# Performance work log

Hardware: AMD Instinct MI355X
Metric: run time of the kernel (lower is better)

The kernel has to match this reference:

```python
import jax, jax.numpy as jnp
import numpy as np

IN_DIM = 64
OUT_DIM = 16  # SPD matrix side
HIDDEN = [128, 128]
CHOL_DIM = OUT_DIM + OUT_DIM * (OUT_DIM - 1) // 2  # 136
BATCH = 65536
LEAKY_SLOPE = 0.01  # torch.nn.LeakyReLU default


def _uniform(key, shape, in_feat):
    b = 1.0 / in_feat
    return jax.random.uniform(key, shape, jnp.float32, -b, b)


def setup_inputs() -> dict:
    key = jax.random.key(0)
    ks = jax.random.split(key, 7)
    x = jax.random.normal(ks[0], (BATCH, IN_DIM), jnp.float32)
    # layer sizes: 64 -> 128 -> 128 -> 136, init uniform(-1/in_feat, 1/in_feat)
    W1 = _uniform(ks[1], (IN_DIM, HIDDEN[0]), IN_DIM)
    b1 = _uniform(ks[2], (HIDDEN[0],), IN_DIM)
    W2 = _uniform(ks[3], (HIDDEN[0], HIDDEN[1]), HIDDEN[0])
    b2 = _uniform(ks[4], (HIDDEN[1],), HIDDEN[0])
    W3 = _uniform(ks[5], (HIDDEN[1], CHOL_DIM), HIDDEN[1])
    b3 = _uniform(ks[6], (CHOL_DIM,), HIDDEN[1])
    return {"x": x, "W1": W1, "b1": b1, "W2": W2, "b2": b2, "W3": W3, "b3": b3}


def reference(x, W1, b1, W2, b2, W3, b3):
    # MLP with LeakyReLU between layers, then Tanh on final output
    h = jax.nn.leaky_relu(x @ W1 + b1, LEAKY_SLOPE)
    h = jax.nn.leaky_relu(h @ W2 + b2, LEAKY_SLOPE)
    ldata = jnp.tanh(h @ W3 + b3)  # [B, 136]

    # fill_tril: scatter the 136 values into the lower triangle (row-major)
    rows, cols = jnp.tril_indices(OUT_DIM)
    L = jnp.zeros((x.shape[0], OUT_DIM, OUT_DIM), x.dtype).at[:, rows, cols].set(ldata)
    Q = L + jnp.swapaxes(L, -1, -2)  # symmetric [B, 16, 16]

    # symmetric eigendecomposition (ascending eigenvalues, like torch.symeig)
    w, V = jnp.linalg.eigh(Q)
    # sqrt(softmax(exp(w)**2)) ; exp(w)**2 == exp(2w)
    ev = jnp.sqrt(jax.nn.softmax(jnp.exp(2.0 * w), axis=-1))  # [B, 16]
    # faithful to source: uses inverse (== V^T in exact math since V orthogonal)
    Vinv = jnp.linalg.inv(V)
    # V @ diag(ev) @ V^{-1}
    return jnp.einsum('bij,bj,bjk->bik', V, ev, Vinv)
```

## Files before the change

kernel.cpp:

```cpp
#include <hip/hip_runtime.h>
#include <math.h>

typedef _Float16 f16;
typedef _Float16 half4_t __attribute__((ext_vector_type(4)));
typedef _Float16 half8_t __attribute__((ext_vector_type(8)));
typedef float floatx4 __attribute__((ext_vector_type(4)));

#define LDATA_OFF_BYTES 86016

__global__ __launch_bounds__(256) void prep_weights(
    const float* __restrict__ W1, const float* __restrict__ W2,
    const float* __restrict__ W3, f16* __restrict__ wt) {
  int t = blockIdx.x * 256 + threadIdx.x;
  if (t < 8192) {
    int c = t >> 6, k = t & 63;
    wt[t] = (f16)W1[k * 128 + c];
  } else if (t < 24576) {
    int u = t - 8192;
    int c = u >> 7, k = u & 127;
    wt[t] = (f16)W2[k * 128 + c];
  } else if (t < 43008) {
    int u = t - 24576;
    int c = u >> 7, k = u & 127;
    wt[t] = (f16)((c < 136) ? W3[k * 136 + c] : 0.0f);
  }
}

__device__ __forceinline__ float fast_tanh(float v) {
  float e = __builtin_amdgcn_exp2f(v * 2.885390081777926814f);
  return 1.0f - 2.0f * __builtin_amdgcn_rcpf(e + 1.0f);
}

__global__ __launch_bounds__(256) void mlp_kernel(
    const float* __restrict__ x, const float* __restrict__ b1,
    const float* __restrict__ b2v, const float* __restrict__ b3,
    const f16* __restrict__ wt, f16* __restrict__ ldata) {
  __shared__ f16 hb[2][4][16][136];
  const int tid = threadIdx.x;
  const int wave = tid >> 6;
  const int lane = tid & 63;
  const int cl = lane & 15;
  const int q = lane >> 4;
  const int r0 = blockIdx.x * 64 + wave * 16;

  const f16* w1t = wt;
  const f16* w2t = wt + 8192;
  const f16* w3t = wt + 24576;

  half8_t a0, a1;
  {
    const float* xr = x + (size_t)(r0 + cl) * 64 + q * 8;
    floatx4 v0 = *(const floatx4*)(xr);
    floatx4 v1 = *(const floatx4*)(xr + 4);
    floatx4 v2 = *(const floatx4*)(xr + 32);
    floatx4 v3 = *(const floatx4*)(xr + 36);
#pragma unroll
    for (int i = 0; i < 4; ++i) {
      a0[i] = (f16)v0[i]; a0[i + 4] = (f16)v1[i];
      a1[i] = (f16)v2[i]; a1[i + 4] = (f16)v3[i];
    }
  }
#pragma unroll
  for (int c8 = 0; c8 < 8; ++c8) {
    int c = c8 * 16 + cl;
    half8_t w0 = *(const half8_t*)(w1t + c * 64 + q * 8);
    half8_t w1v = *(const half8_t*)(w1t + c * 64 + 32 + q * 8);
    floatx4 acc = {0.f, 0.f, 0.f, 0.f};
    acc = __builtin_amdgcn_mfma_f32_16x16x32_f16(a0, w0, acc, 0, 0, 0);
    acc = __builtin_amdgcn_mfma_f32_16x16x32_f16(a1, w1v, acc, 0, 0, 0);
    float bias = b1[c];
#pragma unroll
    for (int i = 0; i < 4; ++i) {
      float v = acc[i] + bias;
      v = v > 0.f ? v : 0.01f * v;
      hb[0][wave][q * 4 + i][c] = (f16)v;
    }
  }
  __syncthreads();

  half8_t ha[4];
#pragma unroll
  for (int ks = 0; ks < 4; ++ks)
    ha[ks] = *(const half8_t*)(&hb[0][wave][cl][ks * 32 + q * 8]);
#pragma unroll
  for (int c8 = 0; c8 < 8; ++c8) {
    int c = c8 * 16 + cl;
    floatx4 acc = {0.f, 0.f, 0.f, 0.f};
#pragma unroll
    for (int ks = 0; ks < 4; ++ks) {
      half8_t wv = *(const half8_t*)(w2t + c * 128 + ks * 32 + q * 8);
      acc = __builtin_amdgcn_mfma_f32_16x16x32_f16(ha[ks], wv, acc, 0, 0, 0);
    }
    float bias = b2v[c];
#pragma unroll
    for (int i = 0; i < 4; ++i) {
      float v = acc[i] + bias;
      v = v > 0.f ? v : 0.01f * v;
      hb[1][wave][q * 4 + i][c] = (f16)v;
    }
  }
  __syncthreads();

#pragma unroll
  for (int ks = 0; ks < 4; ++ks)
    ha[ks] = *(const half8_t*)(&hb[1][wave][cl][ks * 32 + q * 8]);
#pragma unroll
  for (int c8 = 0; c8 < 9; ++c8) {
    int c = c8 * 16 + cl;
    floatx4 acc = {0.f, 0.f, 0.f, 0.f};
#pragma unroll
    for (int ks = 0; ks < 4; ++ks) {
      half8_t wv = *(const half8_t*)(w3t + c * 128 + ks * 32 + q * 8);
      acc = __builtin_amdgcn_mfma_f32_16x16x32_f16(ha[ks], wv, acc, 0, 0, 0);
    }
    if (c < 136) {
      float bias = b3[c];
#pragma unroll
      for (int i = 0; i < 4; ++i)
        ldata[(size_t)(r0 + q * 4 + i) * 136 + c] = (f16)fast_tanh(acc[i] + bias);
    }
  }
}

template <int CTRL>
__device__ __forceinline__ float dpp_add(float v) {
  int t = __builtin_amdgcn_update_dpp(0, __builtin_bit_cast(int, v), CTRL,
                                      0xf, 0xf, true);
  return v + __builtin_bit_cast(float, t);
}
__device__ __forceinline__ float wsum(float v) {
  v = dpp_add<0x111>(v);
  v = dpp_add<0x112>(v);
  v = dpp_add<0x114>(v);
  v = dpp_add<0x118>(v);
  v = dpp_add<0x142>(v);
  v = dpp_add<0x143>(v);
  return __builtin_bit_cast(
      float, __builtin_amdgcn_readlane(__builtin_bit_cast(int, v), 63));
}

__device__ __forceinline__ half4_t to_h(floatx4 v) {
  auto p0 = __builtin_amdgcn_cvt_pkrtz(v[0], v[1]);
  auto p1 = __builtin_amdgcn_cvt_pkrtz(v[2], v[3]);
  half4_t h;
  h[0] = p0[0]; h[1] = p0[1]; h[2] = p1[0]; h[3] = p1[1];
  return h;
}

__device__ __forceinline__ floatx4 expm_c(floatx4 b, floatx4 I4, float& m) {
  float s2 = wsum(b[0] * b[0] + b[1] * b[1] + b[2] * b[2] + b[3] * b[3]);
  float td = wsum(I4[0] * b[0] + I4[1] * b[1] + I4[2] * b[2] + I4[3] * b[3]);
  m = td * 0.0625f;
  float fr2 = fmaxf(s2 - td * m, 1e-30f);
  int e2 = (int)(__builtin_bit_cast(unsigned, fr2) >> 23) - 127;
  int s = (e2 + 5) >> 1;
  s = s < 0 ? 0 : (s > 12 ? 12 : s);
  s = __builtin_amdgcn_readfirstlane(s);
  float sc = __builtin_bit_cast(float, (unsigned)(127 - s) << 23);
  b = (b - I4 * m) * sc;
  half4_t bh = to_h(b);
  floatx4 zero = {0.f, 0.f, 0.f, 0.f};
  floatx4 a2 = __builtin_amdgcn_mfma_f32_16x16x16f16(bh, bh, zero, 0, 0, 0);
  floatx4 t = I4 * 0.5f + b * (1.f / 6.f) + a2 * (1.f / 24.f);
  floatx4 p = __builtin_amdgcn_mfma_f32_16x16x16f16(to_h(a2), to_h(t), I4 + b,
                                                    0, 0, 0);
  for (int k = 0; k < s; ++k) {
    half4_t ph = to_h(p);
    p = __builtin_amdgcn_mfma_f32_16x16x16f16(ph, ph, zero, 0, 0, 0);
  }
  return p;
}

__global__ __launch_bounds__(256) void expm_kernel(
    const f16* __restrict__ ldata, float* __restrict__ out) {
  const int lane = threadIdx.x & 63;
  const int mat = (int)((blockIdx.x * 256u + threadIdx.x) >> 6);
  const int r = lane & 15, q = lane >> 4;
  const f16* ld = ldata + (size_t)mat * 136;

  floatx4 b, I4;
#pragma unroll
  for (int i = 0; i < 4; ++i) {
    int k = q * 4 + i;
    int hi = r > k ? r : k;
    int lo = r + k - hi;
    float v = (float)ld[hi * (hi + 1) / 2 + lo];
    bool d = (r == k);
    I4[i] = d ? 1.f : 0.f;
    b[i] = d ? 4.f * v : 2.f * v;
  }

  float m1;
  floatx4 p = expm_c(b, I4, m1);
  float fac = __builtin_amdgcn_exp2f(m1 * 1.4426950408889634f - 1.0f);
  float m2;
  p = expm_c(p * fac, I4, m2);

  float n2 = wsum(p[0] * p[0] + p[1] * p[1] + p[2] * p[2] + p[3] * p[3]);
  float inv = __builtin_amdgcn_rsqf(n2);
  floatx4 o = p * inv;
  *(floatx4*)(out + (size_t)mat * 256 + r * 16 + q * 4) = o;
}

extern "C" void kernel_launch(void* const* d_in, const int* in_sizes, int n_in,
                              void* d_out, int out_size, void* d_ws,
                              size_t ws_size, hipStream_t stream) {
  const float* x = (const float*)d_in[0];
  const float* W1 = (const float*)d_in[1];
  const float* b1 = (const float*)d_in[2];
  const float* W2 = (const float*)d_in[3];
  const float* b2 = (const float*)d_in[4];
  const float* W3 = (const float*)d_in[5];
  const float* b3 = (const float*)d_in[6];
  float* out = (float*)d_out;
  f16* wt = (f16*)d_ws;
  f16* ldata = (f16*)((char*)d_ws + LDATA_OFF_BYTES);

  prep_weights<<<168, 256, 0, stream>>>(W1, W2, W3, wt);
  mlp_kernel<<<1024, 256, 0, stream>>>(x, b1, b2, b3, wt, ldata);
  expm_kernel<<<16384, 256, 0, stream>>>(ldata, out);
}
```

Before: 148.9 us.

## Keep MLP weights in registers and loop each wave over four row tiles

The MLP kernel now runs one wave per block. That wave keeps the W2/W3 fragments and biases in registers and processes four 16-row tiles in a loop, prefetching the next tile's x. Activations go through a small XOR-swizzled LDS buffer, with no block barriers, to avoid bank conflicts. This removes repeated global/L2 weight loads per tile, at the cost of very high register pressure (68 half8 fragments) and lower occupancy with only 1024 single-wave blocks.

```diff
diff --git a/kernel.cpp b/kernel.cpp
--- a/kernel.cpp
+++ b/kernel.cpp
@@ -31,93 +31,126 @@
   return 1.0f - 2.0f * __builtin_amdgcn_rcpf(e + 1.0f);
 }
 
-__global__ __launch_bounds__(256) void mlp_kernel(
+__global__ __launch_bounds__(64, 1) void mlp_kernel(
     const float* __restrict__ x, const float* __restrict__ b1,
     const float* __restrict__ b2v, const float* __restrict__ b3,
     const f16* __restrict__ wt, f16* __restrict__ ldata) {
-  __shared__ f16 hb[2][4][16][136];
-  const int tid = threadIdx.x;
-  const int wave = tid >> 6;
-  const int lane = tid & 63;
+  __shared__ f16 act[2048];
+  const int lane = threadIdx.x & 63;
   const int cl = lane & 15;
   const int q = lane >> 4;
-  const int r0 = blockIdx.x * 64 + wave * 16;
-
   const f16* w1t = wt;
   const f16* w2t = wt + 8192;
   const f16* w3t = wt + 24576;
 
-  half8_t a0, a1;
-  {
-    const float* xr = x + (size_t)(r0 + cl) * 64 + q * 8;
-    floatx4 v0 = *(const floatx4*)(xr);
-    floatx4 v1 = *(const floatx4*)(xr + 4);
-    floatx4 v2 = *(const floatx4*)(xr + 32);
-    floatx4 v3 = *(const floatx4*)(xr + 36);
+  half8_t w2f[32], w3f[36];
+#pragma unroll
+  for (int c8 = 0; c8 < 8; ++c8) {
+    int c = c8 * 16 + cl;
+#pragma unroll
+    for (int ks = 0; ks < 4; ++ks)
+      w2f[c8 * 4 + ks] = *(const half8_t*)(w2t + c * 128 + ks * 32 + q * 8);
+  }
+#pragma unroll
+  for (int c8 = 0; c8 < 9; ++c8) {
+    int c = c8 * 16 + cl;
+#pragma unroll
+    for (int ks = 0; ks < 4; ++ks)
+      w3f[c8 * 4 + ks] = *(const half8_t*)(w3t + c * 128 + ks * 32 + q * 8);
+  }
+  float bb1[8], bb2[8], bb3[9];
+#pragma unroll
+  for (int c8 = 0; c8 < 8; ++c8) {
+    bb1[c8] = b1[c8 * 16 + cl];
+    bb2[c8] = b2v[c8 * 16 + cl];
+    bb3[c8] = b3[c8 * 16 + cl];
+  }
+  bb3[8] = (cl < 8) ? b3[128 + cl] : 0.f;
+
+  const int tile0 = blockIdx.x * 4;
+  const float* xp = x + (size_t)(tile0 * 16 + cl) * 64 + q * 8;
+  floatx4 v0 = *(const floatx4*)xp;
+  floatx4 v1 = *(const floatx4*)(xp + 4);
+  floatx4 v2 = *(const floatx4*)(xp + 32);
+  floatx4 v3 = *(const floatx4*)(xp + 36);
+
+  for (int t = 0; t < 4; ++t) {
+    const int r0 = (tile0 + t) * 16;
+    half8_t a0, a1;
 #pragma unroll
     for (int i = 0; i < 4; ++i) {
       a0[i] = (f16)v0[i]; a0[i + 4] = (f16)v1[i];
       a1[i] = (f16)v2[i]; a1[i + 4] = (f16)v3[i];
     }
-  }
-#pragma unroll
-  for (int c8 = 0; c8 < 8; ++c8) {
-    int c = c8 * 16 + cl;
-    half8_t w0 = *(const half8_t*)(w1t + c * 64 + q * 8);
-    half8_t w1v = *(const half8_t*)(w1t + c * 64 + 32 + q * 8);
-    floatx4 acc = {0.f, 0.f, 0.f, 0.f};
-    acc = __builtin_amdgcn_mfma_f32_16x16x32_f16(a0, w0, acc, 0, 0, 0);
-    acc = __builtin_amdgcn_mfma_f32_16x16x32_f16(a1, w1v, acc, 0, 0, 0);
-    float bias = b1[c];
-#pragma unroll
-    for (int i = 0; i < 4; ++i) {
-      float v = acc[i] + bias;
-      v = v > 0.f ? v : 0.01f * v;
-      hb[0][wave][q * 4 + i][c] = (f16)v;
-    }
-  }
-  __syncthreads();
-
-  half8_t ha[4];
-#pragma unroll
-  for (int ks = 0; ks < 4; ++ks)
-    ha[ks] = *(const half8_t*)(&hb[0][wave][cl][ks * 32 + q * 8]);
-#pragma unroll
-  for (int c8 = 0; c8 < 8; ++c8) {
-    int c = c8 * 16 + cl;
-    floatx4 acc = {0.f, 0.f, 0.f, 0.f};
-#pragma unroll
-    for (int ks = 0; ks < 4; ++ks) {
-      half8_t wv = *(const half8_t*)(w2t + c * 128 + ks * 32 + q * 8);
-      acc = __builtin_amdgcn_mfma_f32_16x16x32_f16(ha[ks], wv, acc, 0, 0, 0);
-    }
-    float bias = b2v[c];
-#pragma unroll
-    for (int i = 0; i < 4; ++i) {
-      float v = acc[i] + bias;
-      v = v > 0.f ? v : 0.01f * v;
-      hb[1][wave][q * 4 + i][c] = (f16)v;
-    }
-  }
-  __syncthreads();
-
-#pragma unroll
-  for (int ks = 0; ks < 4; ++ks)
-    ha[ks] = *(const half8_t*)(&hb[1][wave][cl][ks * 32 + q * 8]);
-#pragma unroll
-  for (int c8 = 0; c8 < 9; ++c8) {
-    int c = c8 * 16 + cl;
-    floatx4 acc = {0.f, 0.f, 0.f, 0.f};
-#pragma unroll
-    for (int ks = 0; ks < 4; ++ks) {
-      half8_t wv = *(const half8_t*)(w3t + c * 128 + ks * 32 + q * 8);
-      acc = __builtin_amdgcn_mfma_f32_16x16x32_f16(ha[ks], wv, acc, 0, 0, 0);
-    }
-    if (c < 136) {
-      float bias = b3[c];
-#pragma unroll
-      for (int i = 0; i < 4; ++i)
-        ldata[(size_t)(r0 + q * 4 + i) * 136 + c] = (f16)fast_tanh(acc[i] + bias);
+    if (t < 3) {
+      xp = x + (size_t)((tile0 + t + 1) * 16 + cl) * 64 + q * 8;
+      v0 = *(const floatx4*)xp;
+      v1 = *(const floatx4*)(xp + 4);
+      v2 = *(const floatx4*)(xp + 32);
+      v3 = *(const floatx4*)(xp + 36);
+    }
+
+#pragma unroll
+    for (int c8 = 0; c8 < 8; ++c8) {
+      int c = c8 * 16 + cl;
+      half8_t u0 = *(const half8_t*)(w1t + c * 64 + q * 8);
+      half8_t u1 = *(const half8_t*)(w1t + c * 64 + 32 + q * 8);
+      floatx4 acc = {0.f, 0.f, 0.f, 0.f};
+      acc = __builtin_amdgcn_mfma_f32_16x16x32_f16(a0, u0, acc, 0, 0, 0);
+      acc = __builtin_amdgcn_mfma_f32_16x16x32_f16(a1, u1, acc, 0, 0, 0);
+#pragma unroll
+      for (int i = 0; i < 4; ++i) {
+        float v = acc[i] + bb1[c8];
+        v = v > 0.f ? v : 0.01f * v;
+        int row = q * 4 + i;
+        int gs = ((c8 * 2 + (cl >> 3)) ^ row) & 15;
+        act[row * 128 + gs * 8 + (cl & 7)] = (f16)v;
+      }
+    }
+
+    half8_t ha[4];
+#pragma unroll
+    for (int ks = 0; ks < 4; ++ks)
+      ha[ks] = *(const half8_t*)(act + cl * 128 +
+                                 ((((ks << 2) | q) ^ (cl & 15)) << 3));
+
+#pragma unroll
+    for (int c8 = 0; c8 < 8; ++c8) {
+      floatx4 acc = {0.f, 0.f, 0.f, 0.f};
+#pragma unroll
+      for (int ks = 0; ks < 4; ++ks)
+        acc = __builtin_amdgcn_mfma_f32_16x16x32_f16(ha[ks], w2f[c8 * 4 + ks],
+                                                     acc, 0, 0, 0);
+      int c = c8 * 16 + cl;
+#pragma unroll
+      for (int i = 0; i < 4; ++i) {
+        float v = acc[i] + bb2[c8];
+        v = v > 0.f ? v : 0.01f * v;
+        int row = q * 4 + i;
+        int gs = ((c8 * 2 + (cl >> 3)) ^ row) & 15;
+        act[row * 128 + gs * 8 + (cl & 7)] = (f16)v;
+      }
+    }
+
+#pragma unroll
+    for (int ks = 0; ks < 4; ++ks)
+      ha[ks] = *(const half8_t*)(act + cl * 128 +
+                                 ((((ks << 2) | q) ^ (cl & 15)) << 3));
+
+#pragma unroll
+    for (int c8 = 0; c8 < 9; ++c8) {
+      floatx4 acc = {0.f, 0.f, 0.f, 0.f};
+#pragma unroll
+      for (int ks = 0; ks < 4; ++ks)
+        acc = __builtin_amdgcn_mfma_f32_16x16x32_f16(ha[ks], w3f[c8 * 4 + ks],
+                                                     acc, 0, 0, 0);
+      int c = c8 * 16 + cl;
+      if (c < 136) {
+#pragma unroll
+        for (int i = 0; i < 4; ++i)
+          ldata[(size_t)(r0 + q * 4 + i) * 136 + c] =
+              (f16)fast_tanh(acc[i] + bb3[c8]);
+      }
     }
   }
 }
@@ -217,6 +250,6 @@
   f16* ldata = (f16*)((char*)d_ws + LDATA_OFF_BYTES);
 
   prep_weights<<<168, 256, 0, stream>>>(W1, W2, W3, wt);
-  mlp_kernel<<<1024, 256, 0, stream>>>(x, b1, b2, b3, wt, ldata);
+  mlp_kernel<<<1024, 64, 0, stream>>>(x, b1, b2, b3, wt, ldata);
   expm_kernel<<<16384, 256, 0, stream>>>(ldata, out);
 }
```

Result: faster. 130.9 us (-12.0%).
